# Kernel optimization log

Measured on AMD Instinct MI355X. Metric: run time of the kernel, lower is better.

## Reference

```python
import jax, jax.numpy as jnp
import numpy as np

N_NODES = 100000
N_EDGES = 2500000
IN_CH = 32
HID = 16
OUT_CH = 32


def setup_inputs() -> dict:
    key = jax.random.key(0)
    ks = jax.random.split(key, 10)
    x = jax.random.normal(ks[0], (N_NODES, IN_CH), dtype=jnp.float32)
    edge_index = jax.random.randint(ks[1], (2, N_EDGES), 0, N_NODES, dtype=jnp.int64)
    # conv1 MLP: Linear(in,16) -> ReLU -> Linear(16,out)
    W1 = jax.random.normal(ks[2], (IN_CH, HID), dtype=jnp.float32) / np.sqrt(IN_CH)
    b1 = jnp.zeros((HID,), dtype=jnp.float32)
    W2 = jax.random.normal(ks[3], (HID, OUT_CH), dtype=jnp.float32) / np.sqrt(HID)
    b2 = jnp.zeros((OUT_CH,), dtype=jnp.float32)
    # conv2 MLP: Linear(out,16) -> ReLU -> Linear(16,out)
    W3 = jax.random.normal(ks[4], (OUT_CH, HID), dtype=jnp.float32) / np.sqrt(OUT_CH)
    b3 = jnp.zeros((HID,), dtype=jnp.float32)
    W4 = jax.random.normal(ks[5], (HID, OUT_CH), dtype=jnp.float32) / np.sqrt(HID)
    b4 = jnp.zeros((OUT_CH,), dtype=jnp.float32)
    return {"x": x, "edge_index": edge_index, "W1": W1, "b1": b1, "W2": W2,
            "b2": b2, "W3": W3, "b3": b3, "W4": W4, "b4": b4}


def _gin_conv(x, src, dst, W_a, b_a, W_b, b_b):
    # GINConv (eps=0): nn((1+eps)*x + sum_{j in N(i)} x_j)
    agg = jax.ops.segment_sum(x[src], dst, num_segments=x.shape[0])  # [N, d]
    h = x + agg
    h = jnp.maximum(h @ W_a + b_a, 0.0)  # Linear -> ReLU
    return h @ W_b + b_b                 # Linear


def reference(x, edge_index, W1, b1, W2, b2, W3, b3, W4, b4):
    src, dst = edge_index[0], edge_index[1]
    h = _gin_conv(x, src, dst, W1, b1, W2, b2)
    h = jnp.maximum(h, 0.0)  # F.relu between convs
    out = _gin_conv(h, src, dst, W3, b3, W4, b4)
    return out
```

## Files before the change

### kernel.cpp

```cpp
#include <hip/hip_runtime.h>

typedef unsigned short ushort_t;
typedef unsigned int uint_t;

#define BKT_SHIFT 8
#define BKT_NODES 256
#define NBKT_MAX 400
#define BCAP 8192
#define EPB 8192
#define NPB16 64
#define SCOL_N16 2560

__device__ __forceinline__ ushort_t f2bf(float f) {
    unsigned u = __float_as_uint(f);
    unsigned r = (u + 0x7FFFu + ((u >> 16) & 1u)) >> 16;
    return (ushort_t)r;
}
__device__ __forceinline__ float bflo(uint_t u) { return __uint_as_float(u << 16); }
__device__ __forceinline__ float bfhi(uint_t u) { return __uint_as_float(u & 0xFFFF0000u); }

__global__ __launch_bounds__(512) void scatter_lin(
    const int* __restrict__ src, const int* __restrict__ dst,
    int* __restrict__ gcnt, int* __restrict__ staged,
    const float4* __restrict__ x4, const float* __restrict__ W,
    ushort_t* __restrict__ z, int E, int SBLK, int N, int NBKT)
{
    __shared__ float sW[512];
    __shared__ int lcnt[NBKT_MAX];
    __shared__ int lbase[NBKT_MAX];
    __shared__ int lcur[NBKT_MAX];
    int t = threadIdx.x, blk = blockIdx.x;
    if (blk < SBLK) {
        for (int b = t; b < NBKT; b += 512) { lcnt[b] = 0; lcur[b] = 0; }
        __syncthreads();
        int e0 = blk * EPB;
        int rd[16], rs[16];
        #pragma unroll
        for (int i = 0; i < 16; ++i) {
            int e = e0 + i * 512 + t;
            bool ok = (e < E);
            rd[i] = ok ? dst[e] : -1;
            rs[i] = ok ? src[e] : 0;
            if (ok) atomicAdd(&lcnt[rd[i] >> BKT_SHIFT], 1);
        }
        __syncthreads();
        for (int b = t; b < NBKT; b += 512)
            lbase[b] = atomicAdd(&gcnt[b], lcnt[b]);
        __syncthreads();
        #pragma unroll
        for (int i = 0; i < 16; ++i) {
            if (rd[i] >= 0) {
                int b = rd[i] >> BKT_SHIFT;
                int r = lbase[b] + atomicAdd(&lcur[b], 1);
                if (r < BCAP)
                    staged[(size_t)b * BCAP + r] =
                        ((rd[i] & (BKT_NODES - 1)) << 24) | rs[i];
            }
        }
    } else {
        sW[t] = W[t];
        __syncthreads();
        int n = (blk - SBLK) * 512 + t;
        if (n >= N) return;
        float a[16];
        #pragma unroll
        for (int c = 0; c < 16; ++c) a[c] = 0.f;
        const float4* xr = x4 + (size_t)n * 8;
        #pragma unroll
        for (int k4 = 0; k4 < 8; ++k4) {
            float4 xv = xr[k4];
            #pragma unroll
            for (int c = 0; c < 16; ++c) {
                a[c] += xv.x * sW[(k4 * 4 + 0) * 16 + c];
                a[c] += xv.y * sW[(k4 * 4 + 1) * 16 + c];
                a[c] += xv.z * sW[(k4 * 4 + 2) * 16 + c];
                a[c] += xv.w * sW[(k4 * 4 + 3) * 16 + c];
            }
        }
        uint_t w[8];
        #pragma unroll
        for (int i2 = 0; i2 < 8; ++i2)
            w[i2] = (uint_t)f2bf(a[2 * i2]) | ((uint_t)f2bf(a[2 * i2 + 1]) << 16);
        uint4* zo = (uint4*)(z + (size_t)n * 16);
        uint4 q0; q0.x = w[0]; q0.y = w[1]; q0.z = w[2]; q0.w = w[3];
        uint4 q1; q1.x = w[4]; q1.y = w[5]; q1.z = w[6]; q1.w = w[7];
        zo[0] = q0;
        zo[1] = q1;
    }
}

__global__ __launch_bounds__(512) void fine_fill(
    const int* __restrict__ staged, const int* __restrict__ gcnt,
    int2* __restrict__ rp2, int* __restrict__ col,
    int N, int NBKT, int q1, int q2, int q3)
{
    __shared__ int scnt[1024];
    __shared__ int srel[1024];
    __shared__ int scur[1024];
    __shared__ int swsum[256];
    __shared__ int scol[BCAP];
    int b = blockIdx.x, t = threadIdx.x;
    int n0 = b << BKT_SHIFT;
    int nn = min(BKT_NODES, N - n0);
    int e0 = b * BCAP;
    int m = min(gcnt[b], BCAP);

    for (int i = t; i < 1024; i += 512) { scnt[i] = 0; scur[i] = 0; }
    __syncthreads();
    for (int i = t; i < m; i += 512) {
        int v = staged[e0 + i];
        int dl = ((unsigned)v) >> 24;
        int s = v & 0xFFFFFF;
        int q = (s >= q2) ? ((s >= q3) ? 3 : 2) : ((s >= q1) ? 1 : 0);
        atomicAdd(&scnt[dl * 4 + q], 1);
    }
    __syncthreads();
    int c0 = 0, c1 = 0, c2 = 0, c3 = 0, tot = 0;
    if (t < 256) {
        c0 = scnt[t * 4 + 0]; c1 = scnt[t * 4 + 1];
        c2 = scnt[t * 4 + 2]; c3 = scnt[t * 4 + 3];
        tot = c0 + c1 + c2 + c3;
        swsum[t] = tot;
    }
    __syncthreads();
    for (int off = 1; off < 256; off <<= 1) {
        int add = (t < 256 && t >= off) ? swsum[t - off] : 0;
        __syncthreads();
        if (t < 256) swsum[t] += add;
        __syncthreads();
    }
    if (t < 256) {
        int excl = swsum[t] - tot;
        srel[t * 4 + 0] = excl;
        srel[t * 4 + 1] = excl + c0;
        srel[t * 4 + 2] = excl + c0 + c1;
        srel[t * 4 + 3] = excl + c0 + c1 + c2;
        if (t < nn) rp2[n0 + t] = make_int2(e0 + excl, e0 + excl + tot);
    }
    __syncthreads();

    for (int i = t; i < m; i += 512) {
        int v = staged[e0 + i];
        int dl = ((unsigned)v) >> 24;
        int s = v & 0xFFFFFF;
        int q = (s >= q2) ? ((s >= q3) ? 3 : 2) : ((s >= q1) ? 1 : 0);
        int p = srel[dl * 4 + q] + atomicAdd(&scur[dl * 4 + q], 1);
        scol[p] = s;
    }
    __syncthreads();
    for (int i = t; i < m; i += 512) col[e0 + i] = scol[i];
}


template <bool CHAIN>
__global__ __launch_bounds__(256) void agg_mlp16(
    const ushort_t* __restrict__ zin, const int2* __restrict__ rp2,
    const int* __restrict__ col,
    const float* __restrict__ ba,
    const float* __restrict__ Wb, const float* __restrict__ bb,
    const float* __restrict__ Wc,
    void* __restrict__ outv, int N)
{
    __shared__ float sWb[16 * 32];
    __shared__ float sWc[32 * 16];
    __shared__ float sba[16], sbb[32];
    __shared__ float sh[NPB16 * 17];
    __shared__ float sr[NPB16 * 33];
    __shared__ int scol[SCOL_N16];

    int t = threadIdx.x;
    sWb[t] = Wb[t];  sWb[t + 256] = Wb[t + 256];
    if (CHAIN) { sWc[t] = Wc[t];  sWc[t + 256] = Wc[t + 256]; }
    if (t < 16) sba[t] = ba[t];
    if (t < 32) sbb[t] = bb[t];

    int base = blockIdx.x * NPB16;
    int last = min(base + NPB16, N) - 1;
    int kb = rp2[base].x;
    int kt = rp2[last].y;
    int tot = kt - kb;
    bool ovf = (tot > SCOL_N16);
    if (!ovf) {
        for (int i = t; i < tot; i += 256)
            scol[i] = __builtin_nontemporal_load(col + kb + i);
    }
    __syncthreads();

    int ln = t >> 2;
    int sl = t & 3;
    int n  = base + ln;
    bool act = (n < N);
    const uint2* zp = (const uint2*)zin;

    if (act) {
        uint2 us = zp[(size_t)n * 4 + sl];
        float v0 = bflo(us.x), v1 = bfhi(us.x), v2 = bflo(us.y), v3 = bfhi(us.y);
        int2 r = rp2[n];
        int ks = r.x, ke = r.y;
        if (!ovf) {
            int k = ks - kb, kend = ke - kb;
            for (; k + 8 <= kend; k += 8) {
                int s0 = scol[k + 0], s1 = scol[k + 1], s2 = scol[k + 2], s3 = scol[k + 3];
                int s4 = scol[k + 4], s5 = scol[k + 5], s6 = scol[k + 6], s7 = scol[k + 7];
                uint2 u0 = zp[(size_t)s0 * 4 + sl];
                uint2 u1 = zp[(size_t)s1 * 4 + sl];
                uint2 u2 = zp[(size_t)s2 * 4 + sl];
                uint2 u3 = zp[(size_t)s3 * 4 + sl];
                uint2 u4 = zp[(size_t)s4 * 4 + sl];
                uint2 u5 = zp[(size_t)s5 * 4 + sl];
                uint2 u6 = zp[(size_t)s6 * 4 + sl];
                uint2 u7 = zp[(size_t)s7 * 4 + sl];
                v0 += ((bflo(u0.x) + bflo(u1.x)) + (bflo(u2.x) + bflo(u3.x)))
                    + ((bflo(u4.x) + bflo(u5.x)) + (bflo(u6.x) + bflo(u7.x)));
                v1 += ((bfhi(u0.x) + bfhi(u1.x)) + (bfhi(u2.x) + bfhi(u3.x)))
                    + ((bfhi(u4.x) + bfhi(u5.x)) + (bfhi(u6.x) + bfhi(u7.x)));
                v2 += ((bflo(u0.y) + bflo(u1.y)) + (bflo(u2.y) + bflo(u3.y)))
                    + ((bflo(u4.y) + bflo(u5.y)) + (bflo(u6.y) + bflo(u7.y)));
                v3 += ((bfhi(u0.y) + bfhi(u1.y)) + (bfhi(u2.y) + bfhi(u3.y)))
                    + ((bfhi(u4.y) + bfhi(u5.y)) + (bfhi(u6.y) + bfhi(u7.y)));
            }
            for (; k < kend; ++k) {
                uint2 u = zp[(size_t)scol[k] * 4 + sl];
                v0 += bflo(u.x); v1 += bfhi(u.x); v2 += bflo(u.y); v3 += bfhi(u.y);
            }
        } else {
            for (int k = ks; k < ke; ++k) {
                uint2 u = zp[(size_t)col[k] * 4 + sl];
                v0 += bflo(u.x); v1 += bfhi(u.x); v2 += bflo(u.y); v3 += bfhi(u.y);
            }
        }
        int cb = sl * 4;
        sh[ln * 17 + cb + 0] = fmaxf(v0 + sba[cb + 0], 0.f);
        sh[ln * 17 + cb + 1] = fmaxf(v1 + sba[cb + 1], 0.f);
        sh[ln * 17 + cb + 2] = fmaxf(v2 + sba[cb + 2], 0.f);
        sh[ln * 17 + cb + 3] = fmaxf(v3 + sba[cb + 3], 0.f);
    }
    __syncthreads();

    if (act) {
        int c0 = sl * 8;
        float o[8];
        #pragma unroll
        for (int j = 0; j < 8; ++j) o[j] = sbb[c0 + j];
        #pragma unroll
        for (int j = 0; j < 16; ++j) {
            float hj = sh[ln * 17 + j];
            #pragma unroll
            for (int cc = 0; cc < 8; ++cc)
                o[cc] += hj * sWb[j * 32 + c0 + cc];
        }
        if (CHAIN) {
            #pragma unroll
            for (int cc = 0; cc < 8; ++cc)
                sr[ln * 33 + c0 + cc] = fmaxf(o[cc], 0.f);
        } else {
            float* op = (float*)outv + (size_t)n * 32 + c0;
            #pragma unroll
            for (int cc = 0; cc < 8; ++cc)
                __builtin_nontemporal_store(o[cc], op + cc);
        }
    }
    if (CHAIN) {
        __syncthreads();
        if (act) {
            int c0 = sl * 4;
            float a0 = 0.f, a1 = 0.f, a2 = 0.f, a3 = 0.f;
            #pragma unroll
            for (int j = 0; j < 32; ++j) {
                float rj = sr[ln * 33 + j];
                a0 += rj * sWc[j * 16 + c0 + 0];
                a1 += rj * sWc[j * 16 + c0 + 1];
                a2 += rj * sWc[j * 16 + c0 + 2];
                a3 += rj * sWc[j * 16 + c0 + 3];
            }
            uint_t p0 = (uint_t)f2bf(a0) | ((uint_t)f2bf(a1) << 16);
            uint_t p1 = (uint_t)f2bf(a2) | ((uint_t)f2bf(a3) << 16);
            uint_t* op = (uint_t*)outv + (size_t)n * 8 + sl * 2;
            op[0] = p0;
            op[1] = p1;
        }
    }
}


extern "C" void kernel_launch(void* const* d_in, const int* in_sizes, int n_in,
                              void* d_out, int out_size, void* d_ws, size_t ws_size,
                              hipStream_t stream) {
    const float* x  = (const float*)d_in[0];
    const int*   ei = (const int*)d_in[1];
    const float* W1 = (const float*)d_in[2];
    const float* b1 = (const float*)d_in[3];
    const float* W2 = (const float*)d_in[4];
    const float* b2 = (const float*)d_in[5];
    const float* W3 = (const float*)d_in[6];
    const float* b3 = (const float*)d_in[7];
    const float* W4 = (const float*)d_in[8];
    const float* b4 = (const float*)d_in[9];

    const int N = in_sizes[0] / 32;
    const int E = in_sizes[1] / 2;
    const int* src = ei;
    const int* dst = ei + E;

    const int NBKT = (N + BKT_NODES - 1) >> BKT_SHIFT;
    const int SBLK = (E + EPB - 1) / EPB;
    const int LINB = (N + 511) / 512;

    char* ws = (char*)d_ws;
    size_t o = 0;
    auto alloc = [&](size_t bytes) -> char* {
        o = (o + 255) & ~(size_t)255;
        char* r = ws + o;
        o += bytes;
        return r;
    };
    int*      gcnt   = (int*)     alloc(4 * (size_t)NBKT);
    int*      staged = (int*)     alloc(4 * (size_t)NBKT * BCAP);
    int*      col    = (int*)     alloc(4 * (size_t)NBKT * BCAP);
    int2*     rp2    = (int2*)    alloc(8 * (size_t)N);
    ushort_t* zb     = (ushort_t*)alloc(2 * (size_t)N * 16);
    ushort_t* z2b    = (ushort_t*)alloc(2 * (size_t)N * 16);

    hipMemsetAsync(gcnt, 0, 4 * (size_t)NBKT, stream);

    scatter_lin<<<SBLK + LINB, 512, 0, stream>>>(
        src, dst, gcnt, staged, (const float4*)x, W1, zb, E, SBLK, N, NBKT);

    int q1 = N / 4, q2 = N / 2, q3 = (3 * N) / 4;
    fine_fill<<<NBKT, 512, 0, stream>>>(staged, gcnt, rp2, col, N, NBKT, q1, q2, q3);

    agg_mlp16<true ><<<(N + NPB16 - 1) / NPB16, 256, 0, stream>>>(
        zb, rp2, col, b1, W2, b2, W3, z2b, N);
    agg_mlp16<false><<<(N + NPB16 - 1) / NPB16, 256, 0, stream>>>(
        z2b, rp2, col, b3, W4, b4, nullptr, d_out, N);
}
```

Measured before the change: 177.4 us.

## Fuse per-bucket CSR sort into aggregation kernels and shrink buckets to 64 nodes

Drops the separate fine_fill kernel that built rp2/col arrays. Each aggregation block now reads its 64-node bucket of staged edges, counting-sorts them in shared memory by destination and low source bits, then aggregates directly. This removes one launch and the col/rp2 global write/read, at the cost of redoing the sort in both conv passes. It also changes the source sub-ordering from quartile ranges to low bits (v&3), which may reduce gather locality. The smaller BCAP of 2560 edges per bucket means edges beyond that are dropped if a bucket overflows.

```diff
diff --git a/kernel.cpp b/kernel.cpp
--- a/kernel.cpp
+++ b/kernel.cpp
@@ -3,13 +3,11 @@
 typedef unsigned short ushort_t;
 typedef unsigned int uint_t;
 
-#define BKT_SHIFT 8
-#define BKT_NODES 256
-#define NBKT_MAX 400
-#define BCAP 8192
+#define BKT_SHIFT 6
+#define BKT_NODES 64
+#define NBKT_MAX 1600
+#define BCAP 2560
 #define EPB 8192
-#define NPB16 64
-#define SCOL_N16 2560
 
 __device__ __forceinline__ ushort_t f2bf(float f) {
     unsigned u = __float_as_uint(f);
@@ -89,73 +87,11 @@
     }
 }
 
-__global__ __launch_bounds__(512) void fine_fill(
-    const int* __restrict__ staged, const int* __restrict__ gcnt,
-    int2* __restrict__ rp2, int* __restrict__ col,
-    int N, int NBKT, int q1, int q2, int q3)
-{
-    __shared__ int scnt[1024];
-    __shared__ int srel[1024];
-    __shared__ int scur[1024];
-    __shared__ int swsum[256];
-    __shared__ int scol[BCAP];
-    int b = blockIdx.x, t = threadIdx.x;
-    int n0 = b << BKT_SHIFT;
-    int nn = min(BKT_NODES, N - n0);
-    int e0 = b * BCAP;
-    int m = min(gcnt[b], BCAP);
-
-    for (int i = t; i < 1024; i += 512) { scnt[i] = 0; scur[i] = 0; }
-    __syncthreads();
-    for (int i = t; i < m; i += 512) {
-        int v = staged[e0 + i];
-        int dl = ((unsigned)v) >> 24;
-        int s = v & 0xFFFFFF;
-        int q = (s >= q2) ? ((s >= q3) ? 3 : 2) : ((s >= q1) ? 1 : 0);
-        atomicAdd(&scnt[dl * 4 + q], 1);
-    }
-    __syncthreads();
-    int c0 = 0, c1 = 0, c2 = 0, c3 = 0, tot = 0;
-    if (t < 256) {
-        c0 = scnt[t * 4 + 0]; c1 = scnt[t * 4 + 1];
-        c2 = scnt[t * 4 + 2]; c3 = scnt[t * 4 + 3];
-        tot = c0 + c1 + c2 + c3;
-        swsum[t] = tot;
-    }
-    __syncthreads();
-    for (int off = 1; off < 256; off <<= 1) {
-        int add = (t < 256 && t >= off) ? swsum[t - off] : 0;
-        __syncthreads();
-        if (t < 256) swsum[t] += add;
-        __syncthreads();
-    }
-    if (t < 256) {
-        int excl = swsum[t] - tot;
-        srel[t * 4 + 0] = excl;
-        srel[t * 4 + 1] = excl + c0;
-        srel[t * 4 + 2] = excl + c0 + c1;
-        srel[t * 4 + 3] = excl + c0 + c1 + c2;
-        if (t < nn) rp2[n0 + t] = make_int2(e0 + excl, e0 + excl + tot);
-    }
-    __syncthreads();
-
-    for (int i = t; i < m; i += 512) {
-        int v = staged[e0 + i];
-        int dl = ((unsigned)v) >> 24;
-        int s = v & 0xFFFFFF;
-        int q = (s >= q2) ? ((s >= q3) ? 3 : 2) : ((s >= q1) ? 1 : 0);
-        int p = srel[dl * 4 + q] + atomicAdd(&scur[dl * 4 + q], 1);
-        scol[p] = s;
-    }
-    __syncthreads();
-    for (int i = t; i < m; i += 512) col[e0 + i] = scol[i];
-}
-
 
 template <bool CHAIN>
-__global__ __launch_bounds__(256) void agg_mlp16(
-    const ushort_t* __restrict__ zin, const int2* __restrict__ rp2,
-    const int* __restrict__ col,
+__global__ __launch_bounds__(256) void agg_sort_mlp(
+    const ushort_t* __restrict__ zin, const int* __restrict__ staged,
+    const int* __restrict__ gcnt,
     const float* __restrict__ ba,
     const float* __restrict__ Wb, const float* __restrict__ bb,
     const float* __restrict__ Wc,
@@ -164,70 +100,93 @@
     __shared__ float sWb[16 * 32];
     __shared__ float sWc[32 * 16];
     __shared__ float sba[16], sbb[32];
-    __shared__ float sh[NPB16 * 17];
-    __shared__ float sr[NPB16 * 33];
-    __shared__ int scol[SCOL_N16];
+    __shared__ float sh[BKT_NODES * 17];
+    __shared__ float sr[BKT_NODES * 33];
+    __shared__ int scnt[256];
+    __shared__ int srel[256];
+    __shared__ int scur[256];
+    __shared__ int snode[BKT_NODES + 1];
+    __shared__ int scol[BCAP];
 
     int t = threadIdx.x;
     sWb[t] = Wb[t];  sWb[t + 256] = Wb[t + 256];
     if (CHAIN) { sWc[t] = Wc[t];  sWc[t + 256] = Wc[t + 256]; }
     if (t < 16) sba[t] = ba[t];
     if (t < 32) sbb[t] = bb[t];
-
-    int base = blockIdx.x * NPB16;
-    int last = min(base + NPB16, N) - 1;
-    int kb = rp2[base].x;
-    int kt = rp2[last].y;
-    int tot = kt - kb;
-    bool ovf = (tot > SCOL_N16);
-    if (!ovf) {
-        for (int i = t; i < tot; i += 256)
-            scol[i] = __builtin_nontemporal_load(col + kb + i);
+    scnt[t] = 0;  scur[t] = 0;
+    __syncthreads();
+
+    int b = blockIdx.x;
+    int m = min(gcnt[b], BCAP);
+    const int* sp = staged + (size_t)b * BCAP;
+
+    for (int i = t; i < m; i += 256) {
+        int v = sp[i];
+        atomicAdd(&scnt[(((unsigned)v >> 24) << 2) | (v & 3)], 1);
+    }
+    __syncthreads();
+
+    if (t < 64) {
+        int c0 = scnt[t * 4 + 0], c1 = scnt[t * 4 + 1];
+        int c2 = scnt[t * 4 + 2], c3 = scnt[t * 4 + 3];
+        int tot = c0 + c1 + c2 + c3;
+        int sc = tot;
+        #pragma unroll
+        for (int off = 1; off < 64; off <<= 1) {
+            int up = __shfl_up(sc, off, 64);
+            if (t >= off) sc += up;
+        }
+        int excl = sc - tot;
+        snode[t] = excl;
+        if (t == 63) snode[64] = sc;
+        srel[t * 4 + 0] = excl;
+        srel[t * 4 + 1] = excl + c0;
+        srel[t * 4 + 2] = excl + c0 + c1;
+        srel[t * 4 + 3] = excl + c0 + c1 + c2;
+    }
+    __syncthreads();
+
+    for (int i = t; i < m; i += 256) {
+        int v = sp[i];
+        int idx = (((unsigned)v >> 24) << 2) | (v & 3);
+        int p = srel[idx] + atomicAdd(&scur[idx], 1);
+        scol[p] = v & 0xFFFFFF;
     }
     __syncthreads();
 
     int ln = t >> 2;
     int sl = t & 3;
-    int n  = base + ln;
+    int n  = (b << BKT_SHIFT) + ln;
     bool act = (n < N);
     const uint2* zp = (const uint2*)zin;
 
     if (act) {
         uint2 us = zp[(size_t)n * 4 + sl];
         float v0 = bflo(us.x), v1 = bfhi(us.x), v2 = bflo(us.y), v3 = bfhi(us.y);
-        int2 r = rp2[n];
-        int ks = r.x, ke = r.y;
-        if (!ovf) {
-            int k = ks - kb, kend = ke - kb;
-            for (; k + 8 <= kend; k += 8) {
-                int s0 = scol[k + 0], s1 = scol[k + 1], s2 = scol[k + 2], s3 = scol[k + 3];
-                int s4 = scol[k + 4], s5 = scol[k + 5], s6 = scol[k + 6], s7 = scol[k + 7];
-                uint2 u0 = zp[(size_t)s0 * 4 + sl];
-                uint2 u1 = zp[(size_t)s1 * 4 + sl];
-                uint2 u2 = zp[(size_t)s2 * 4 + sl];
-                uint2 u3 = zp[(size_t)s3 * 4 + sl];
-                uint2 u4 = zp[(size_t)s4 * 4 + sl];
-                uint2 u5 = zp[(size_t)s5 * 4 + sl];
-                uint2 u6 = zp[(size_t)s6 * 4 + sl];
-                uint2 u7 = zp[(size_t)s7 * 4 + sl];
-                v0 += ((bflo(u0.x) + bflo(u1.x)) + (bflo(u2.x) + bflo(u3.x)))
-                    + ((bflo(u4.x) + bflo(u5.x)) + (bflo(u6.x) + bflo(u7.x)));
-                v1 += ((bfhi(u0.x) + bfhi(u1.x)) + (bfhi(u2.x) + bfhi(u3.x)))
-                    + ((bfhi(u4.x) + bfhi(u5.x)) + (bfhi(u6.x) + bfhi(u7.x)));
-                v2 += ((bflo(u0.y) + bflo(u1.y)) + (bflo(u2.y) + bflo(u3.y)))
-                    + ((bflo(u4.y) + bflo(u5.y)) + (bflo(u6.y) + bflo(u7.y)));
-                v3 += ((bfhi(u0.y) + bfhi(u1.y)) + (bfhi(u2.y) + bfhi(u3.y)))
-                    + ((bfhi(u4.y) + bfhi(u5.y)) + (bfhi(u6.y) + bfhi(u7.y)));
-            }
-            for (; k < kend; ++k) {
-                uint2 u = zp[(size_t)scol[k] * 4 + sl];
-                v0 += bflo(u.x); v1 += bfhi(u.x); v2 += bflo(u.y); v3 += bfhi(u.y);
-            }
-        } else {
-            for (int k = ks; k < ke; ++k) {
-                uint2 u = zp[(size_t)col[k] * 4 + sl];
-                v0 += bflo(u.x); v1 += bfhi(u.x); v2 += bflo(u.y); v3 += bfhi(u.y);
-            }
+        int k = snode[ln], kend = snode[ln + 1];
+        for (; k + 8 <= kend; k += 8) {
+            int s0 = scol[k + 0], s1 = scol[k + 1], s2 = scol[k + 2], s3 = scol[k + 3];
+            int s4 = scol[k + 4], s5 = scol[k + 5], s6 = scol[k + 6], s7 = scol[k + 7];
+            uint2 u0 = zp[(size_t)s0 * 4 + sl];
+            uint2 u1 = zp[(size_t)s1 * 4 + sl];
+            uint2 u2 = zp[(size_t)s2 * 4 + sl];
+            uint2 u3 = zp[(size_t)s3 * 4 + sl];
+            uint2 u4 = zp[(size_t)s4 * 4 + sl];
+            uint2 u5 = zp[(size_t)s5 * 4 + sl];
+            uint2 u6 = zp[(size_t)s6 * 4 + sl];
+            uint2 u7 = zp[(size_t)s7 * 4 + sl];
+            v0 += ((bflo(u0.x) + bflo(u1.x)) + (bflo(u2.x) + bflo(u3.x)))
+                + ((bflo(u4.x) + bflo(u5.x)) + (bflo(u6.x) + bflo(u7.x)));
+            v1 += ((bfhi(u0.x) + bfhi(u1.x)) + (bfhi(u2.x) + bfhi(u3.x)))
+                + ((bfhi(u4.x) + bfhi(u5.x)) + (bfhi(u6.x) + bfhi(u7.x)));
+            v2 += ((bflo(u0.y) + bflo(u1.y)) + (bflo(u2.y) + bflo(u3.y)))
+                + ((bflo(u4.y) + bflo(u5.y)) + (bflo(u6.y) + bflo(u7.y)));
+            v3 += ((bfhi(u0.y) + bfhi(u1.y)) + (bfhi(u2.y) + bfhi(u3.y)))
+                + ((bfhi(u4.y) + bfhi(u5.y)) + (bfhi(u6.y) + bfhi(u7.y)));
+        }
+        for (; k < kend; ++k) {
+            uint2 u = zp[(size_t)scol[k] * 4 + sl];
+            v0 += bflo(u.x); v1 += bfhi(u.x); v2 += bflo(u.y); v3 += bfhi(u.y);
         }
         int cb = sl * 4;
         sh[ln * 17 + cb + 0] = fmaxf(v0 + sba[cb + 0], 0.f);
@@ -316,8 +275,6 @@
     };
     int*      gcnt   = (int*)     alloc(4 * (size_t)NBKT);
     int*      staged = (int*)     alloc(4 * (size_t)NBKT * BCAP);
-    int*      col    = (int*)     alloc(4 * (size_t)NBKT * BCAP);
-    int2*     rp2    = (int2*)    alloc(8 * (size_t)N);
     ushort_t* zb     = (ushort_t*)alloc(2 * (size_t)N * 16);
     ushort_t* z2b    = (ushort_t*)alloc(2 * (size_t)N * 16);
 
@@ -326,11 +283,8 @@
     scatter_lin<<<SBLK + LINB, 512, 0, stream>>>(
         src, dst, gcnt, staged, (const float4*)x, W1, zb, E, SBLK, N, NBKT);
 
-    int q1 = N / 4, q2 = N / 2, q3 = (3 * N) / 4;
-    fine_fill<<<NBKT, 512, 0, stream>>>(staged, gcnt, rp2, col, N, NBKT, q1, q2, q3);
-
-    agg_mlp16<true ><<<(N + NPB16 - 1) / NPB16, 256, 0, stream>>>(
-        zb, rp2, col, b1, W2, b2, W3, z2b, N);
-    agg_mlp16<false><<<(N + NPB16 - 1) / NPB16, 256, 0, stream>>>(
-        z2b, rp2, col, b3, W4, b4, nullptr, d_out, N);
-}
+    agg_sort_mlp<true ><<<NBKT, 256, 0, stream>>>(
+        zb, staged, gcnt, b1, W2, b2, W3, z2b, N);
+    agg_sort_mlp<false><<<NBKT, 256, 0, stream>>>(
+        z2b, staged, gcnt, b3, W4, b4, nullptr, d_out, N);
+}
```

Result: no change. 177.4 us (-0.0%).
